# Kernel optimization log

Hardware: AMD Instinct MI355X
Metric: run time of the kernel (lower is better)

## Reference

```python
import jax, jax.numpy as jnp
import numpy as np

N_QUBITS = 10
SAMPLE_LENGTH = 2 ** N_QUBITS  # AmplitudeEmbedding requires len(features) == 2**n
NUM_CLASSES = 10
BATCH = 8192
TOTAL_PARAMS = N_QUBITS + 12 * (N_QUBITS // 2) * 2 + N_QUBITS * 3  # 160
C64 = jnp.complex64

H_GATE = (jnp.array([[1, 1], [1, -1]], dtype=C64) * np.float32(1.0 / np.sqrt(2.0)))
CNOT = jnp.array([[1, 0, 0, 0], [0, 1, 0, 0], [0, 0, 0, 1], [0, 0, 1, 0]], dtype=C64)
CZ = jnp.diag(jnp.array([1, 1, 1, -1], dtype=C64))


def rx(t):
    c = jnp.cos(t / 2).astype(C64)
    s = jnp.sin(t / 2).astype(C64)
    return jnp.stack([jnp.stack([c, -1j * s]), jnp.stack([-1j * s, c])])


def ry(t):
    c = jnp.cos(t / 2).astype(C64)
    s = jnp.sin(t / 2).astype(C64)
    return jnp.stack([jnp.stack([c, -s]), jnp.stack([s, c])])


def rz(t):
    e = jnp.exp(-0.5j * t).astype(C64)
    z = jnp.zeros_like(e)
    return jnp.stack([jnp.stack([e, z]), jnp.stack([z, jnp.conj(e)])])


def rot(phi, theta, omega):
    # qml.Rot = RZ(omega) @ RY(theta) @ RZ(phi)
    return rz(omega) @ ry(theta) @ rz(phi)


def apply_gate(psi, U, wires):
    # psi: (B, 2, 2, ..., 2); U: (2**k, 2**k); wires in PennyLane order (wire 0 = MSB = axis 1)
    k = len(wires)
    U = U.reshape((2,) * (2 * k))
    axes = [1 + w for w in wires]
    psi = jnp.tensordot(U, psi, axes=(list(range(k, 2 * k)), axes))
    return jnp.moveaxis(psi, list(range(k)), axes)


def vqc_block(psi, p, i):
    psi = apply_gate(psi, rx(p[0]), [i])
    psi = apply_gate(psi, ry(p[1]), [i + 1])
    psi = apply_gate(psi, ry(p[2]), [i])
    psi = apply_gate(psi, rz(p[3]), [i + 1])
    psi = apply_gate(psi, rz(p[4]), [i])
    psi = apply_gate(psi, rx(p[5]), [i + 1])
    psi = apply_gate(psi, CZ, [i, i + 1])
    psi = apply_gate(psi, rz(p[6]), [i])
    psi = apply_gate(psi, rx(p[7]), [i + 1])
    psi = apply_gate(psi, ry(p[8]), [i])
    psi = apply_gate(psi, rz(p[9]), [i + 1])
    psi = apply_gate(psi, rx(p[10]), [i])
    psi = apply_gate(psi, ry(p[11]), [i + 1])
    psi = apply_gate(psi, CNOT, [i + 1, i])
    return psi


def circuit(x, all_params):
    n = N_QUBITS
    B = x.shape[0]
    # AmplitudeEmbedding with normalize=True
    norm = jnp.linalg.norm(x, axis=1, keepdims=True)
    psi = (x / norm).astype(C64).reshape((B,) + (2,) * n)
    emb = all_params[:n]
    v1 = all_params[n:n + 12 * (n // 2)].reshape(n // 2, 12)
    v2 = all_params[n + 12 * (n // 2):n + 24 * (n // 2)].reshape(n // 2, 12)
    sel = all_params[n + 24 * (n // 2):].reshape(n, 3)
    # embedding layer: H then RY on each wire
    for i in range(n):
        psi = apply_gate(psi, H_GATE, [i])
    for i in range(n):
        psi = apply_gate(psi, ry(emb[i]), [i])
    # two stacks of VQC blocks on even wire pairs
    for i in range(n // 2):
        psi = vqc_block(psi, v1[i], 2 * i)
    for i in range(n // 2):
        psi = vqc_block(psi, v2[i], 2 * i)
    # CNOT ring
    for i in range(n):
        psi = apply_gate(psi, CNOT, [i, (i + 1) % n])
    # StronglyEntanglingLayers, 1 layer: Rot on each wire, then CNOT ring (range=1)
    for i in range(n):
        psi = apply_gate(psi, rot(sel[i, 0], sel[i, 1], sel[i, 2]), [i])
    for i in range(n):
        psi = apply_gate(psi, CNOT, [i, (i + 1) % n])
    # <Z_i> = sum_s |psi_s|^2 * (1 - 2*bit_i(s)), wire 0 = MSB
    probs = (jnp.abs(psi) ** 2).reshape(B, 2 ** n)
    bits = (jnp.arange(2 ** n)[None, :] >> (n - 1 - jnp.arange(n))[:, None]) & 1
    signs = (1 - 2 * bits).astype(jnp.float32)  # (n, 2**n)
    return probs @ signs.T  # (B, n)


def setup_inputs() -> dict:
    key = jax.random.key(0)
    ks = jax.random.split(key, 4)
    x = jax.random.normal(ks[0], (BATCH, SAMPLE_LENGTH), dtype=jnp.float32)
    all_params = jax.random.normal(ks[1], (TOTAL_PARAMS,), dtype=jnp.float32)
    w_in = jax.random.normal(ks[2], (N_QUBITS, SAMPLE_LENGTH), dtype=jnp.float32) * np.float32(1.0 / np.sqrt(SAMPLE_LENGTH))
    b_in = jnp.zeros((N_QUBITS,), dtype=jnp.float32)
    w_fc = jax.random.normal(ks[3], (NUM_CLASSES, N_QUBITS), dtype=jnp.float32) * np.float32(1.0 / np.sqrt(N_QUBITS))
    b_fc = jnp.zeros((NUM_CLASSES,), dtype=jnp.float32)
    return {"x": x, "all_params": all_params, "w_in": w_in, "b_in": b_in, "w_fc": w_fc, "b_fc": b_fc}


def reference(x, all_params, w_in, b_in, w_fc, b_fc):
    x_proj = x @ w_in.T + b_in          # (B, n_qubits)
    q_out = circuit(x, all_params)      # (B, n_qubits)
    q_out = q_out + x_proj              # residual add (dropout is identity at eval)
    return q_out @ w_fc.T + b_fc        # (B, num_classes)
```

## Files before the change

### kernel.cpp

```cpp
#include <hip/hip_runtime.h>

typedef __attribute__((ext_vector_type(2))) float f2;

#define WAIT_LDS asm volatile("s_waitcnt lgkmcnt(0)" ::: "memory")

__device__ __forceinline__ f2 mk(float a, float b){ f2 r; r.x=a; r.y=b; return r; }

__device__ __forceinline__ void cmadS(f2& c, f2 g, f2 b){
  asm("v_pk_fma_f32 %0, %1, %2, %0 op_sel:[0,0,0] op_sel_hi:[0,1,1]\n\t"
      "v_pk_fma_f32 %0, %1, %2, %0 op_sel:[1,1,0] op_sel_hi:[1,0,1] neg_lo:[1,0,0]"
      : "+v"(c) : "s"(g), "v"(b));
}
__device__ __forceinline__ f2 cmulS(f2 g, f2 b){
  f2 d;
  asm("v_pk_mul_f32 %0, %1, %2 op_sel:[0,0] op_sel_hi:[0,1]\n\t"
      "v_pk_fma_f32 %0, %1, %2, %0 op_sel:[1,1,0] op_sel_hi:[1,0,1] neg_lo:[1,0,0]"
      : "=&v"(d) : "s"(g), "v"(b));
  return d;
}
__device__ __forceinline__ void quadS(const f2* __restrict__ G, f2& a0, f2& a1, f2& a2, f2& a3){
  f2 c0,c1,c2,c3;
  c0=cmulS(G[0],a0);  c1=cmulS(G[1],a0);  c2=cmulS(G[2],a0);  c3=cmulS(G[3],a0);
  cmadS(c0,G[4],a1);  cmadS(c1,G[5],a1);  cmadS(c2,G[6],a1);  cmadS(c3,G[7],a1);
  cmadS(c0,G[8],a2);  cmadS(c1,G[9],a2);  cmadS(c2,G[10],a2); cmadS(c3,G[11],a2);
  cmadS(c0,G[12],a3); cmadS(c1,G[13],a3); cmadS(c2,G[14],a3); cmadS(c3,G[15],a3);
  a0=c0; a1=c1; a2=c2; a3=c3;
}

__device__ __forceinline__ float2 cmul(float2 a, float2 b){
  return make_float2(a.x*b.x - a.y*b.y, a.x*b.y + a.y*b.x);
}
__device__ __forceinline__ float2 cmad(float2 acc, float2 a, float2 b){
  acc.x += a.x*b.x - a.y*b.y; acc.y += a.x*b.y + a.y*b.x; return acc;
}

__global__ __launch_bounds__(64) void qm_setup(
    const float* __restrict__ params, const float* __restrict__ w_fc,
    const float* __restrict__ b_in, const float* __restrict__ b_fc,
    float* __restrict__ wsf){
  __shared__ float2 m2[50][4];
  __shared__ float2 h4[10][16];
  const int t = threadIdx.x;

  if (t < 50){
    int typ[5], pix[5], ng;
    if (t < 40){
      int i = t>>3, k = t&7;
      int P1 = 10 + i*12, P2 = 70 + i*12;
      switch(k){
        case 0: ng=5; typ[0]=3;pix[0]=0;     typ[1]=1;pix[1]=2*i;   typ[2]=0;pix[2]=P1+0;
                      typ[3]=1;pix[3]=P1+2;  typ[4]=2;pix[4]=P1+4;  break;
        case 1: ng=5; typ[0]=3;pix[0]=0;     typ[1]=1;pix[1]=2*i+1; typ[2]=1;pix[2]=P1+1;
                      typ[3]=2;pix[3]=P1+3;  typ[4]=0;pix[4]=P1+5;  break;
        case 2: ng=3; typ[0]=2;pix[0]=P1+6;  typ[1]=1;pix[1]=P1+8;  typ[2]=0;pix[2]=P1+10; break;
        case 3: ng=3; typ[0]=0;pix[0]=P1+7;  typ[1]=2;pix[1]=P1+9;  typ[2]=1;pix[2]=P1+11; break;
        case 4: ng=3; typ[0]=0;pix[0]=P2+0;  typ[1]=1;pix[1]=P2+2;  typ[2]=2;pix[2]=P2+4;  break;
        case 5: ng=3; typ[0]=1;pix[0]=P2+1;  typ[1]=2;pix[1]=P2+3;  typ[2]=0;pix[2]=P2+5;  break;
        case 6: ng=3; typ[0]=2;pix[0]=P2+6;  typ[1]=1;pix[1]=P2+8;  typ[2]=0;pix[2]=P2+10; break;
        default:ng=3; typ[0]=0;pix[0]=P2+7;  typ[1]=2;pix[1]=P2+9;  typ[2]=1;pix[2]=P2+11; break;
      }
    } else {
      int S = 130 + (t-40)*3;
      ng=3; typ[0]=2;pix[0]=S+0; typ[1]=1;pix[1]=S+1; typ[2]=2;pix[2]=S+2;
    }
    float2 M[4] = {{1.f,0.f},{0.f,0.f},{0.f,0.f},{1.f,0.f}};
    #pragma clang loop unroll(disable)
    for (int g=0; g<ng; ++g){
      float2 R[4];
      if (typ[g]==3){
        const float r_=0.70710678118654752f;
        R[0]={r_,0.f}; R[1]={r_,0.f}; R[2]={r_,0.f}; R[3]={-r_,0.f};
      } else {
        float th = params[pix[g]]*0.5f;
        float c = cosf(th), s = sinf(th);
        if (typ[g]==0){ R[0]={c,0.f}; R[1]={0.f,-s}; R[2]={0.f,-s}; R[3]={c,0.f}; }
        else if (typ[g]==1){ R[0]={c,0.f}; R[1]={-s,0.f}; R[2]={s,0.f}; R[3]={c,0.f}; }
        else { R[0]={c,-s}; R[1]={0.f,0.f}; R[2]={0.f,0.f}; R[3]={c,s}; }
      }
      float2 T0=cmad(cmul(R[0],M[0]), R[1], M[2]);
      float2 T1=cmad(cmul(R[0],M[1]), R[1], M[3]);
      float2 T2=cmad(cmul(R[2],M[0]), R[3], M[2]);
      float2 T3=cmad(cmul(R[2],M[1]), R[3], M[3]);
      M[0]=T0; M[1]=T1; M[2]=T2; M[3]=T3;
    }
    m2[t][0]=M[0]; m2[t][1]=M[1]; m2[t][2]=M[2]; m2[t][3]=M[3];
  }
  __syncthreads();
  if (t < 10){
    int i = t>>1, L = t&1;
    const float2* A1 = m2[i*8 + L*4 + 0];
    const float2* B1 = m2[i*8 + L*4 + 1];
    const float2* A2 = m2[i*8 + L*4 + 2];
    const float2* B2 = m2[i*8 + L*4 + 3];
    float2 K1[16], K2[16];
    #pragma clang loop unroll(disable)
    for (int r=0;r<4;r++)
      #pragma clang loop unroll(disable)
      for (int c=0;c<4;c++){
        K1[r*4+c] = cmul(A1[(r>>1)*2+(c>>1)], B1[(r&1)*2+(c&1)]);
        K2[r*4+c] = cmul(A2[(r>>1)*2+(c>>1)], B2[(r&1)*2+(c&1)]);
      }
    #pragma clang loop unroll(disable)
    for (int c=0;c<4;c++){ K1[12+c].x=-K1[12+c].x; K1[12+c].y=-K1[12+c].y; }
    #pragma clang loop unroll(disable)
    for (int r=0;r<4;r++){
      int rr = (r==1)?3:(r==3)?1:r;
      #pragma clang loop unroll(disable)
      for (int c=0;c<4;c++){
        float2 v = cmul(K2[r*4+0], K1[0+c]);
        v = cmad(v, K2[r*4+1], K1[4+c]);
        v = cmad(v, K2[r*4+2], K1[8+c]);
        v = cmad(v, K2[r*4+3], K1[12+c]);
        h4[t][rr*4+c] = v;
      }
    }
  }
  __syncthreads();
  if (t < 5){
    const float2* Ga = h4[t*2+1];
    const float2* Gb = h4[t*2+0];
    float2* dst = (float2*)wsf + t*16;
    #pragma clang loop unroll(disable)
    for (int r=0;r<4;r++)
      #pragma clang loop unroll(disable)
      for (int c=0;c<4;c++){
        float2 v = cmul(Ga[r*4+0], Gb[0+c]);
        v = cmad(v, Ga[r*4+1], Gb[4+c]);
        v = cmad(v, Ga[r*4+2], Gb[8+c]);
        v = cmad(v, Ga[r*4+3], Gb[12+c]);
        dst[c*4+r] = v;
      }
  } else if (t < 10){
    int i = t-5;
    const float2* Ra = m2[40 + 2*i];
    const float2* Rb = m2[40 + 2*i + 1];
    float2* dst = (float2*)wsf + 80 + i*16;
    #pragma clang loop unroll(disable)
    for (int r=0;r<4;r++)
      #pragma clang loop unroll(disable)
      for (int c=0;c<4;c++)
        dst[c*4+r] = cmul(Ra[(r>>1)*2+(c>>1)], Rb[(r&1)*2+(c&1)]);
  } else if (t < 20){
    int c = t-10;
    float s = b_fc[c];
    #pragma clang loop unroll(disable)
    for (int q=0;q<10;q++) s += w_fc[c*10+q]*b_in[q];
    wsf[320+c] = s;
  }
}

__global__ __launch_bounds__(256,4) void qm_sim(
    const float* __restrict__ x, const float* __restrict__ w_in,
    const float* __restrict__ w_fc, const float* __restrict__ wsf,
    float* __restrict__ out)
{
  __shared__ __align__(16) f2 psi[4096];
  const int t = threadIdx.x;
  const int l = t & 63, wid = t >> 6;
  const int sample = (blockIdx.x<<2) + wid;
  char* PB = (char*)(psi + (wid<<10));
  const float* xr = x + ((size_t)sample<<10);
  const f2* G = (const f2*)wsf;

  float4 xv0 = *(const float4*)(xr + (l<<4));
  float4 xv1 = *(const float4*)(xr + (l<<4) + 4);
  float4 xv2 = *(const float4*)(xr + (l<<4) + 8);
  float4 xv3 = *(const float4*)(xr + (l<<4) + 12);
  f2 xc[8];
  xc[0]=mk(xv0.x,xv0.y); xc[1]=mk(xv0.z,xv0.w); xc[2]=mk(xv1.x,xv1.y); xc[3]=mk(xv1.z,xv1.w);
  xc[4]=mk(xv2.x,xv2.y); xc[5]=mk(xv2.z,xv2.w); xc[6]=mk(xv3.x,xv3.y); xc[7]=mk(xv3.z,xv3.w);
  f2 xq[5];
  #pragma unroll
  for (int q=0;q<10;q++){
    const float4* wr = (const float4*)(w_in + (q<<10) + (l<<4));
    float4 w0=wr[0], w1=wr[1], w2=wr[2], w3=wr[3];
    f2 a;
    a  = xc[0]*mk(w0.x,w0.y);
    a += xc[1]*mk(w0.z,w0.w);
    a += xc[2]*mk(w1.x,w1.y);
    a += xc[3]*mk(w1.z,w1.w);
    a += xc[4]*mk(w2.x,w2.y);
    a += xc[5]*mk(w2.z,w2.w);
    a += xc[6]*mk(w3.x,w3.y);
    a += xc[7]*mk(w3.z,w3.w);
    float s = a.x + a.y;
    if (q&1) xq[q>>1].y = s; else xq[q>>1].x = s;
  }
  f2 nn = xc[0]*xc[0]; nn += xc[1]*xc[1]; nn += xc[2]*xc[2]; nn += xc[3]*xc[3];
  nn += xc[4]*xc[4]; nn += xc[5]*xc[5]; nn += xc[6]*xc[6]; nn += xc[7]*xc[7];
  float n2 = nn.x + nn.y;
  float xs[16];
  #pragma unroll
  for (int k=0;k<16;k++) xs[k] = xr[(k<<6)|l];
  #pragma unroll
  for (int o=1;o<64;o<<=1) n2 += __shfl_xor(n2, o);
  float rn = rsqrtf(n2);

  f2 A[16];
  #pragma unroll
  for (int k=0;k<16;k++) A[k] = mk(xs[k]*rn, 0.f);
  #pragma unroll
  for (int j=0;j<4;j++) quadS(G+ 0, A[j], A[4+j], A[8+j], A[12+j]);
  #pragma unroll
  for (int i=0;i<4;i++) quadS(G+16, A[4*i], A[4*i+1], A[4*i+2], A[4*i+3]);
  const int Lb = (l ^ (l>>4)) << 3;
  #pragma unroll
  for (int k=0;k<16;k++){
    const int ck = (((k<<6) ^ ((k&3)<<2)) << 3);
    *(f2*)(PB + (Lb ^ ck)) = A[k];
  }
  WAIT_LDS;

  const int L2 = ((((l>>2)<<6)) ^ (l&3) ^ (l&0xC)) << 3;
  #pragma unroll
  for (int k=0;k<16;k++){
    const int ck = (((k<<2) ^ (k>>2)) << 3);
    A[k] = *(const f2*)(PB + (L2 ^ ck));
  }
  #pragma unroll
  for (int j=0;j<4;j++) quadS(G+32, A[j], A[4+j], A[8+j], A[12+j]);
  #pragma unroll
  for (int i=0;i<4;i++) quadS(G+48, A[4*i], A[4*i+1], A[4*i+2], A[4*i+3]);
  #pragma unroll
  for (int k=0;k<16;k++){
    const int ck = (((k<<2) ^ (k>>2)) << 3);
    *(f2*)(PB + (L2 ^ ck)) = A[k];
  }
  WAIT_LDS;

  {
    const int L3 = (((l<<4) ^ (l<<3)) ^ ((l ^ (l>>1)) & 15)) << 3;
    const int IOFF[4] = {0, 0x6, 0xC, 0xA};
    #pragma unroll
    for (int k=0;k<16;k++){
      const int ck = ((IOFF[k>>2] ^ (k&3)) << 3);
      A[k] = *(const f2*)(PB + (L3 ^ ck));
    }
    quadS(G+64, A[0], A[1], A[2], A[3]);
    quadS(G+64, A[6], A[7], A[4], A[5]);
    quadS(G+64, A[8], A[9], A[10], A[11]);
    quadS(G+64, A[14], A[15], A[12], A[13]);
    #pragma unroll
    for (int j=0;j<4;j++) quadS(G+128, A[j], A[4+j], A[8+j], A[12+j]);
    const int L3w = ((l<<4) ^ (l&15)) << 3;
    const int PJ[4] = {0, 0x201, 0x203, 0x002};
    #pragma unroll
    for (int k=0;k<16;k++){
      const int ck = (((k & 0xC) ^ PJ[k&3]) << 3);
      *(f2*)(PB + (L3w ^ ck)) = A[k];
    }
  }
  WAIT_LDS;

  #pragma unroll
  for (int k=0;k<16;k++){
    const int ck = (((k<<6) ^ ((k&3)<<2)) << 3);
    A[k] = *(const f2*)(PB + (Lb ^ ck));
  }
  #pragma unroll
  for (int j=0;j<4;j++) quadS(G+80, A[j], A[4+j], A[8+j], A[12+j]);
  #pragma unroll
  for (int i=0;i<4;i++) quadS(G+96, A[4*i], A[4*i+1], A[4*i+2], A[4*i+3]);
  #pragma unroll
  for (int k=0;k<16;k++){
    const int ck = (((k<<6) ^ ((k&3)<<2)) << 3);
    *(f2*)(PB + (Lb ^ ck)) = A[k];
  }
  WAIT_LDS;

  const int L5 = ((((l>>2)<<6)) ^ ((l&3)<<2) ^ (l&0xC)) << 3;
  #pragma unroll
  for (int k=0;k<16;k++){
    const int ck = ((((k>>2)<<4) ^ (k>>2) ^ (k&3)) << 3);
    A[k] = *(const f2*)(PB + (L5 ^ ck));
  }
  #pragma unroll
  for (int j=0;j<4;j++) quadS(G+112, A[j], A[4+j], A[8+j], A[12+j]);
  #pragma unroll
  for (int i=0;i<4;i++) quadS(G+144, A[4*i], A[4*i+1], A[4*i+2], A[4*i+3]);

  float p[16];
  #pragma unroll
  for (int k=0;k<16;k++){ f2 s = A[k]*A[k]; p[k] = s.x + s.y; }
  {
    int sl = ((l>>2)<<6) | ((l&3)<<2);
    int sc = sl; sc ^= sc>>1; sc ^= sc>>2; sc ^= sc>>4; sc ^= sc>>8;
    int Pl = (sc & 0x1FF) | (((sc ^ (sc>>9)) & 1) << 9);
    float* PF = (float*)PB;
    const int PI[4]  = {0, 0x21F, 0x23F, 0x020};
    const int PJ2[4] = {0, 0x201, 0x203, 0x002};
    #pragma unroll
    for (int k=0;k<16;k++){
      int tgt = Pl ^ PI[k>>2] ^ PJ2[k&3];
      PF[tgt + (tgt>>4)] = p[k];
    }
  }
  WAIT_LDS;

  const float* PR = (const float*)PB + 17*l;
  float q0=PR[0], q1=PR[1], q2=PR[2], q3=PR[3], q4=PR[4], q5=PR[5], q6=PR[6], q7=PR[7];
  float q8=PR[8], q9=PR[9], q10=PR[10], q11=PR[11], q12=PR[12], q13=PR[13], q14=PR[14], q15=PR[15];

  float D[10];
  float s0=q0+q1, s1=q2+q3, s2=q4+q5, s3=q6+q7, s4=q8+q9, s5=q10+q11, s6=q12+q13, s7=q14+q15;
  float d0=q0-q1, d1=q2-q3, d2=q4-q5, d3=q6-q7, d4=q8-q9, d5=q10-q11, d6=q12-q13, d7=q14-q15;
  D[0] = ((d0+d1)+(d2+d3)) + ((d4+d5)+(d6+d7));
  float ss0=s0+s1, ss1=s2+s3, ss2=s4+s5, ss3=s6+s7;
  D[1] = ((s0-s1)+(s2-s3)) + ((s4-s5)+(s6-s7));
  float sss0=ss0+ss1, sss1=ss2+ss3;
  D[2] = (ss0-ss1) + (ss2-ss3);
  D[3] = sss0 - sss1;
  float S_ = sss0 + sss1;
  #pragma unroll
  for (int b=0;b<6;b++){
    const int o = 1<<b;
    float Sp = __shfl_xor(S_, o);
    float dd = S_ - Sp;
    D[4+b] = (l & o) ? -dd : dd;
    S_ += Sp;
    #pragma unroll
    for (int j2=0;j2<4+b;j2++) D[j2] += __shfl_xor(D[j2], o);
  }
  union LL { f2 v; unsigned long long u; };
  #pragma unroll
  for (int k=0;k<5;k++){
    LL z; z.v = xq[k];
    #pragma unroll
    for (int o=1;o<64;o<<=1){ LL w; w.u = __shfl_xor(z.u, o); z.v += w.v; }
    xq[k] = z.v;
  }

  if (l < 10){
    float o = wsf[320+l];
    const float* wf = w_fc + l*10;
    #pragma unroll
    for (int q=0;q<10;q++){
      float xpq = (q&1) ? xq[q>>1].y : xq[q>>1].x;
      o += wf[q] * (D[9-q] + xpq);
    }
    out[(size_t)sample*10 + l] = o;
  }
}

extern "C" void kernel_launch(void* const* d_in, const int* in_sizes, int n_in,
                              void* d_out, int out_size, void* d_ws, size_t ws_size,
                              hipStream_t stream) {
  const float* x      = (const float*)d_in[0];
  const float* params = (const float*)d_in[1];
  const float* w_in   = (const float*)d_in[2];
  const float* b_in   = (const float*)d_in[3];
  const float* w_fc   = (const float*)d_in[4];
  const float* b_fc   = (const float*)d_in[5];
  float* out = (float*)d_out;

  float* wsf = (float*)d_ws;

  int batch = in_sizes[0] >> 10;

  qm_setup<<<dim3(1), dim3(64), 0, stream>>>(params, w_fc, b_in, b_fc, wsf);
  qm_sim<<<dim3(batch>>2), dim3(256), 0, stream>>>(x, w_in, w_fc, wsf, out);
}
```

Before: 59.33 us.

## Replace LDS-staged Z-expectation reduction with in-register Walsh-Hadamard shuffle butterfly

Removes the LDS write/read transpose of the probabilities and computes the per-qubit Z expectations through a butterfly of signed and plain xor-shuffles held in registers, with the outputs relabelled to the new ordering. It also halves the block to 128 threads (2 samples per block) with launch bounds (128,5) and half the shared memory. The intent is to cut an LDS round trip and the long serial shuffle chain, and to schedule smaller blocks more flexibly. The risks are the extra shuffle count and the changed occupancy and register limit.

```diff
diff --git a/kernel.cpp b/kernel.cpp
--- a/kernel.cpp
+++ b/kernel.cpp
@@ -149,15 +149,19 @@
   }
 }
 
-__global__ __launch_bounds__(256,4) void qm_sim(
+#define SGN_IP(V, o) { float t_=__shfl_xor(V,o); float d_=V-t_; V = (l&(o))?-d_:d_; }
+#define PLAIN_IP(V, o) { V += __shfl_xor(V,o); }
+#define SPLIT(Vp, Vs, V, o) { float t_=__shfl_xor(V,o); Vp = V+t_; float d_=V-t_; Vs=(l&(o))?-d_:d_; }
+
+__global__ __launch_bounds__(128,5) void qm_sim(
     const float* __restrict__ x, const float* __restrict__ w_in,
     const float* __restrict__ w_fc, const float* __restrict__ wsf,
     float* __restrict__ out)
 {
-  __shared__ __align__(16) f2 psi[4096];
+  __shared__ __align__(16) f2 psi[2048];
   const int t = threadIdx.x;
   const int l = t & 63, wid = t >> 6;
-  const int sample = (blockIdx.x<<2) + wid;
+  const int sample = (blockIdx.x<<1) + wid;
   char* PB = (char*)(psi + (wid<<10));
   const float* xr = x + ((size_t)sample<<10);
   const f2* G = (const f2*)wsf;
@@ -281,46 +285,33 @@
 
   float p[16];
   #pragma unroll
-  for (int k=0;k<16;k++){ f2 s = A[k]*A[k]; p[k] = s.x + s.y; }
-  {
-    int sl = ((l>>2)<<6) | ((l&3)<<2);
-    int sc = sl; sc ^= sc>>1; sc ^= sc>>2; sc ^= sc>>4; sc ^= sc>>8;
-    int Pl = (sc & 0x1FF) | (((sc ^ (sc>>9)) & 1) << 9);
-    float* PF = (float*)PB;
-    const int PI[4]  = {0, 0x21F, 0x23F, 0x020};
-    const int PJ2[4] = {0, 0x201, 0x203, 0x002};
-    #pragma unroll
-    for (int k=0;k<16;k++){
-      int tgt = Pl ^ PI[k>>2] ^ PJ2[k&3];
-      PF[tgt + (tgt>>4)] = p[k];
-    }
-  }
-  WAIT_LDS;
-
-  const float* PR = (const float*)PB + 17*l;
-  float q0=PR[0], q1=PR[1], q2=PR[2], q3=PR[3], q4=PR[4], q5=PR[5], q6=PR[6], q7=PR[7];
-  float q8=PR[8], q9=PR[9], q10=PR[10], q11=PR[11], q12=PR[12], q13=PR[13], q14=PR[14], q15=PR[15];
-
-  float D[10];
-  float s0=q0+q1, s1=q2+q3, s2=q4+q5, s3=q6+q7, s4=q8+q9, s5=q10+q11, s6=q12+q13, s7=q14+q15;
-  float d0=q0-q1, d1=q2-q3, d2=q4-q5, d3=q6-q7, d4=q8-q9, d5=q10-q11, d6=q12-q13, d7=q14-q15;
-  D[0] = ((d0+d1)+(d2+d3)) + ((d4+d5)+(d6+d7));
-  float ss0=s0+s1, ss1=s2+s3, ss2=s4+s5, ss3=s6+s7;
-  D[1] = ((s0-s1)+(s2-s3)) + ((s4-s5)+(s6-s7));
-  float sss0=ss0+ss1, sss1=ss2+ss3;
-  D[2] = (ss0-ss1) + (ss2-ss3);
-  D[3] = sss0 - sss1;
-  float S_ = sss0 + sss1;
-  #pragma unroll
-  for (int b=0;b<6;b++){
-    const int o = 1<<b;
-    float Sp = __shfl_xor(S_, o);
-    float dd = S_ - Sp;
-    D[4+b] = (l & o) ? -dd : dd;
-    S_ += Sp;
-    #pragma unroll
-    for (int j2=0;j2<4+b;j2++) D[j2] += __shfl_xor(D[j2], o);
-  }
+  for (int k=0;k<16;k++){ f2 sq = A[k]*A[k]; p[k] = sq.x + sq.y; }
+  float sg[4], eg[4], fg[4];
+  #pragma unroll
+  for (int g=0; g<4; ++g){
+    float a_=p[4*g]+p[4*g+1], b_=p[4*g+2]+p[4*g+3];
+    float c_=p[4*g]-p[4*g+1], d_=p[4*g+2]-p[4*g+3];
+    sg[g]=a_+b_; eg[g]=a_-b_; fg[g]=c_-d_;
+  }
+  float s01=sg[0]+sg[1], s23=sg[2]+sg[3];
+  float d01=sg[0]-sg[1], d23=sg[2]-sg[3];
+  float S  = s01+s23;
+  float W8 = s01-s23;
+  float WC = d01-d23;
+  float WE = (eg[0]-eg[1])-(eg[2]-eg[3]);
+  float WF = (fg[0]-fg[1])-(fg[2]-fg[3]);
+  float WCp, WCs, WCpp, WCps, WCss, Sp, Ss, Spp, Sps, q0;
+  PLAIN_IP(S,1); PLAIN_IP(W8,1); SPLIT(WCp, WCs, WC, 1); SGN_IP(WE,1); SGN_IP(WF,1);
+  PLAIN_IP(S,2); PLAIN_IP(W8,2); SPLIT(WCpp, WCps, WCp, 2); SGN_IP(WCs,2); SGN_IP(WE,2); SGN_IP(WF,2);
+  WCss = WCs;
+  SPLIT(Sp, Ss, S, 4); SGN_IP(W8,4); SGN_IP(WCpp,4); SGN_IP(WCps,4); SGN_IP(WCss,4); SGN_IP(WE,4); SGN_IP(WF,4);
+  SPLIT(Spp, Sps, Sp, 8); SGN_IP(Ss,8); SGN_IP(W8,8); SGN_IP(WCpp,8); SGN_IP(WCps,8); SGN_IP(WCss,8); SGN_IP(WE,8); SGN_IP(WF,8);
+  SGN_IP(Spp,16); SGN_IP(Sps,16); SGN_IP(Ss,16); SGN_IP(W8,16); SGN_IP(WCpp,16);
+  SGN_IP(WCps,16); SGN_IP(WCss,16); SGN_IP(WE,16); SGN_IP(WF,16);
+  SGN_IP(Spp,32); SGN_IP(Sps,32); SGN_IP(Ss,32); SGN_IP(W8,32); SGN_IP(WCpp,32);
+  SGN_IP(WCps,32); SGN_IP(WCss,32); SGN_IP(WE,32);
+  { float t_=__shfl_xor(WF,32); q0 = WF+t_; float d_=WF-t_; WF=(l&32)?-d_:d_; }
+
   union LL { f2 v; unsigned long long u; };
   #pragma unroll
   for (int k=0;k<5;k++){
@@ -331,12 +322,13 @@
   }
 
   if (l < 10){
+    float W[10] = {q0, Spp, Sps, Ss, W8, WCpp, WCps, WCss, WE, WF};
     float o = wsf[320+l];
     const float* wf = w_fc + l*10;
     #pragma unroll
     for (int q=0;q<10;q++){
       float xpq = (q&1) ? xq[q>>1].y : xq[q>>1].x;
-      o += wf[q] * (D[9-q] + xpq);
+      o += wf[q] * (W[q] + xpq);
     }
     out[(size_t)sample*10 + l] = o;
   }
@@ -358,5 +350,5 @@
   int batch = in_sizes[0] >> 10;
 
   qm_setup<<<dim3(1), dim3(64), 0, stream>>>(params, w_fc, b_in, b_fc, wsf);
-  qm_sim<<<dim3(batch>>2), dim3(256), 0, stream>>>(x, w_in, w_fc, wsf, out);
-}
+  qm_sim<<<dim3(batch>>1), dim3(128), 0, stream>>>(x, w_in, w_fc, wsf, out);
+}
```

Result: slower. 60.84 us, median of 3 (+2.5%).
